# Kernel tuning notes

Measured on AMD Instinct MI355X. Metric: run time of the kernel, lower is better.

Reference implementation:

```python
import jax, jax.numpy as jnp
import numpy as np

N, E = 50000, 640000
DN, DA, S = 128, 64, 128
MAX_IT, THR = 10, 0.01


def setup_inputs() -> dict:
    key = jax.random.key(0)
    ks = jax.random.split(key, 20)
    inp = {
        'nodes': jax.random.normal(ks[0], (N, DN), jnp.float32),
        'arcs': jax.random.normal(ks[1], (E, 2 + DA), jnp.float32),
        'set_mask': jnp.ones((N,), bool),
        'output_mask': jnp.ones((N,), bool),
        'adj_src': jax.random.randint(ks[2], (E,), 0, N, jnp.int32),
        'adj_dst': jax.random.randint(ks[3], (E,), 0, N, jnp.int32),
        'adj_vals': jax.random.uniform(ks[4], (E,), jnp.float32),
        'an_dst': jax.random.randint(ks[5], (E,), 0, N, jnp.int32),
        'an_vals': jax.random.uniform(ks[6], (E,), jnp.float32),
        'state_init': 0.1 * jax.random.normal(ks[7], (N, S), jnp.float32),
        'Ws1': 0.05 * jax.random.normal(ks[8], (2 * S + 2 * DN + DA, 512), jnp.float32),
        'bs1': jnp.zeros((512,), jnp.float32),
        'Ws2': 0.05 * jax.random.normal(ks[9], (512, S), jnp.float32),
        'bs2': jnp.zeros((S,), jnp.float32),
        'Wo1': 0.05 * jax.random.normal(ks[10], (S + DN, 512), jnp.float32),
        'bo1': jnp.zeros((512,), jnp.float32),
        'Wo2': 0.05 * jax.random.normal(ks[11], (512, 7), jnp.float32),
        'bo2': jnp.zeros((7,), jnp.float32),
    }
    return inp


def _spmm(vals, src, dst, dense, n):
    # sparse [n,n] (or [n,E]) @ dense via gather + segment-sum
    return jax.ops.segment_sum(vals[:, None] * dense[src], dst, num_segments=n)


def reference(nodes, arcs, set_mask, output_mask, adj_src, adj_dst, adj_vals,
              an_dst, an_vals, state_init, Ws1, bs1, Ws2, bs2, Wo1, bo1, Wo2, bo2):
    n = nodes.shape[0]
    arc_labels = arcs[:, 2:]                                   # [E, DA]
    # aggregated_arcs = transposed_arcnode @ arcs[:,2:]  ([N,E] sparse)
    agg_arcs = jax.ops.segment_sum(an_vals[:, None] * arc_labels, an_dst, num_segments=n)
    # aggregated_nodes = transposed_adjacency @ nodes (state_vect_dim > 0 branch)
    agg_nodes = _spmm(adj_vals, adj_src, adj_dst, nodes, n)

    def net_state(x):
        return jnp.tanh(jnp.tanh(x @ Ws1 + bs1) @ Ws2 + bs2)

    def step(carry, _):
        state, state_old, k, done = carry
        dist = jnp.sqrt(jnp.sum(jnp.square(state - state_old), axis=1))
        norm = jnp.sqrt(jnp.sum(jnp.square(state_old), axis=1))
        cont = jnp.logical_and(jnp.any(dist > THR * norm), jnp.logical_not(done))
        agg_states = _spmm(adj_vals, adj_src, adj_dst, state, n)
        inp = jnp.concatenate([state, nodes, agg_states, agg_nodes, agg_arcs], axis=1)
        new_state = net_state(inp)
        state_next = jnp.where(cont, new_state, state)
        state_old_next = jnp.where(cont, state, state_old)
        return (state_next, state_old_next, k + cont.astype(jnp.float32), jnp.logical_not(cont)), None

    init = (state_init, jnp.ones_like(state_init), jnp.float32(0), jnp.array(False))
    (state, _, k, _), _ = jax.lax.scan(step, init, None, length=MAX_IT)

    # apply_filters: concat state|nodes, keep masked rows (mask applied as zeroing to keep static shapes)
    mask = jnp.logical_and(set_mask, output_mask)
    h = jnp.concatenate([state, nodes], axis=1)
    out = jnp.tanh(h @ Wo1 + bo1) @ Wo2 + bo2
    return out * mask[:, None].astype(out.dtype)
```

## Files before the change

kernel.cpp:

```cpp
#include <hip/hip_runtime.h>

typedef unsigned short u16;
typedef unsigned int u32;
typedef __attribute__((ext_vector_type(8))) short short8;
typedef __attribute__((ext_vector_type(4))) float f32x4;

#define THR2 1e-4f

__device__ __forceinline__ u16 f2bf(float f) {
    u32 u = __float_as_uint(f);
    u32 r = u + 0x7fffu + ((u >> 16) & 1u);
    return (u16)(r >> 16);
}
__device__ __forceinline__ float bf2f(u16 h) { return __uint_as_float(((u32)h) << 16); }
__device__ __forceinline__ float lo16(u32 u) { return __uint_as_float(u << 16); }
__device__ __forceinline__ float hi16(u32 u) { return __uint_as_float(u & 0xffff0000u); }

__device__ __forceinline__ void gl_lds16(const u16* g, u16* l) {
    __builtin_amdgcn_global_load_lds(
        (const __attribute__((address_space(1))) void*)g,
        (__attribute__((address_space(3))) void*)l, 16, 0, 0);
}


__global__ void k_zero2(int* a, int* b, int n, int* flags) {
    int i = blockIdx.x * 256 + threadIdx.x;
    if (blockIdx.x == 0 && threadIdx.x < 64) flags[threadIdx.x] = 0;
    if (i < n) { a[i] = 0; b[i] = 0; }
}

__global__ void k_hist2(const int* __restrict__ adst, const int* __restrict__ ndst,
                        int* ca, int* cn, int E) {
    int e = blockIdx.x * 256 + threadIdx.x;
    if (e < E) {
        atomicAdd(&ca[adst[e]], 1);
        atomicAdd(&cn[ndst[e]], 1);
    }
}

__global__ void k_scan_p1(const int* __restrict__ cnt, int* bs, int n) {
    __shared__ int s[256];
    int i = blockIdx.x * 256 + threadIdx.x;
    s[threadIdx.x] = (i < n) ? cnt[i] : 0;
    __syncthreads();
    for (int off = 128; off > 0; off >>= 1) {
        if (threadIdx.x < off) s[threadIdx.x] += s[threadIdx.x + off];
        __syncthreads();
    }
    if (threadIdx.x == 0) bs[blockIdx.x] = s[0];
}

__global__ void k_scan_p2(int* bs, int nb, int* rp, int n) {
    if (threadIdx.x == 0 && blockIdx.x == 0) {
        int run = 0;
        for (int b = 0; b < nb; ++b) { int t = bs[b]; bs[b] = run; run += t; }
        rp[n] = run;
    }
}

__global__ void k_scan_p3(const int* __restrict__ cnt, const int* __restrict__ bs,
                          int* rp, int* cur, int n) {
    __shared__ int s[256];
    int i = blockIdx.x * 256 + threadIdx.x;
    int v = (i < n) ? cnt[i] : 0;
    s[threadIdx.x] = v;
    __syncthreads();
    for (int off = 1; off < 256; off <<= 1) {
        int t = (threadIdx.x >= off) ? s[threadIdx.x - off] : 0;
        __syncthreads();
        s[threadIdx.x] += t;
        __syncthreads();
    }
    int excl = s[threadIdx.x] - v + bs[blockIdx.x];
    if (i < n) { rp[i] = excl; cur[i] = excl; }
}

__global__ void k_fill2(const int* __restrict__ asrc, const int* __restrict__ adst,
                        const float* __restrict__ avals,
                        int* curA, int2* __restrict__ cvA,
                        const int* __restrict__ ndst, const float* __restrict__ nvals,
                        int* curN, int2* __restrict__ cvN, int E) {
    int e = blockIdx.x * 256 + threadIdx.x;
    if (e < E) {
        int p = atomicAdd(&curA[adst[e]], 1);
        long long pa = ((long long)__float_as_int(avals[e]) << 32) | (u32)asrc[e];
        __builtin_nontemporal_store(pa, (long long*)(cvA + p));
        int q = atomicAdd(&curN[ndst[e]], 1);
        long long pn = ((long long)__float_as_int(nvals[e]) << 32) | (u32)e;
        __builtin_nontemporal_store(pn, (long long*)(cvN + q));
    }
}


__global__ void k_pack_all(const float* __restrict__ Ws1, const float* __restrict__ Ws2,
                           const float* __restrict__ Wo1,
                           u16* W1selT, u16* W1baseT, u16* W2T, u16* Wo1T) {
    int i = blockIdx.x * 256 + threadIdx.x;
    if (i < 131072) {
        int n = i >> 8, k = i & 255;
        int r = (k < 128) ? k : k + 128;
        W1selT[i] = f2bf(Ws1[r * 512 + n]);
    } else if (i < 294912) {
        int t = i - 131072;
        int n = t / 320, k = t % 320;
        int r = (k < 128) ? (k + 128) : (k + 256);
        W1baseT[t] = f2bf(Ws1[r * 512 + n]);
    } else if (i < 360448) {
        int t = i - 294912;
        int n = t >> 9, kp = t & 511;
        int q = kp & 63;
        int k = (kp & ~63) + ((q & 3) << 4) + (q >> 2);
        W2T[t] = f2bf(Ws2[k * 128 + n]);
    } else if (i < 491520) {
        int t = i - 360448;
        int n = t >> 8, k = t & 255;
        Wo1T[t] = f2bf(Wo1[k * 512 + n]);
    }
}


__global__ void k_conv_all(const float* __restrict__ nodes, const float* __restrict__ st,
                           u16* X0, u16* SA0, u16* SA2, int N) {
    int i = blockIdx.x * 256 + threadIdx.x;
    int total = N * 32;
    if (i < total) {
        int r = i >> 5, c4 = i & 31;
        float4 f = *(const float4*)(nodes + (size_t)r * 128 + c4 * 4);
        uint2 o;
        o.x = ((u32)f2bf(f.y) << 16) | f2bf(f.x);
        o.y = ((u32)f2bf(f.w) << 16) | f2bf(f.z);
        *(uint2*)(X0 + (size_t)r * 320 + c4 * 4) = o;
    } else if (i < 2 * total) {
        int t = i - total;
        int r = t >> 5, c4 = t & 31;
        float4 f = *(const float4*)(st + (size_t)r * 128 + c4 * 4);
        uint2 o;
        o.x = ((u32)f2bf(f.y) << 16) | f2bf(f.x);
        o.y = ((u32)f2bf(f.w) << 16) | f2bf(f.z);
        *(uint2*)(SA0 + (size_t)r * 256 + c4 * 4) = o;
    } else if (i < 3 * total) {
        int t = i - 2 * total;
        int r = t >> 5, c4 = t & 31;
        uint2 o; o.x = 0x3f803f80u; o.y = 0x3f803f80u;
        *(uint2*)(SA2 + (size_t)r * 256 + c4 * 4) = o;
    }
}

__global__ void k_build_fa(const u16* __restrict__ SA1, const float* __restrict__ nodes,
                           u16* FA, int N) {
    int i = blockIdx.x * 256 + threadIdx.x;
    if (i >= N * 64) return;
    int r = i >> 6, c = i & 63;
    if (c < 32) {
        uint2 o = *(const uint2*)(SA1 + (size_t)r * 256 + c * 4);
        *(uint2*)(FA + (size_t)r * 256 + c * 4) = o;
    } else {
        float4 f = *(const float4*)(nodes + (size_t)r * 128 + (c - 32) * 4);
        uint2 o;
        o.x = ((u32)f2bf(f.y) << 16) | f2bf(f.x);
        o.y = ((u32)f2bf(f.w) << 16) | f2bf(f.z);
        *(uint2*)(FA + (size_t)r * 256 + c * 4) = o;
    }
}


__global__ void k_agg_const(const int* __restrict__ rpA, const int2* __restrict__ cvA,
                            const float* __restrict__ nodes,
                            const int* __restrict__ rpN, const int2* __restrict__ cvN,
                            const float* __restrict__ arcs,
                            u16* X0, int N) {
    int row = blockIdx.x * 4 + (threadIdx.x >> 6);
    if (row >= N) return;
    int l = threadIdx.x & 63;
    int h = l >> 4;
    int lc = l & 15;
    if (blockIdx.y == 0) {
        float b0 = 0.f, b1 = 0.f, b2 = 0.f, b3 = 0.f;
        float b4 = 0.f, b5 = 0.f, b6 = 0.f, b7 = 0.f;
        int s = rpA[row], e = rpA[row + 1];
        int j = s;
        for (; j + 8 <= e; j += 8) {
            int2 p0 = cvA[j + h], p1 = cvA[j + 4 + h];
            const float* r0 = nodes + (size_t)p0.x * 128 + 8 * lc;
            const float* r1 = nodes + (size_t)p1.x * 128 + 8 * lc;
            float4 f0a = *(const float4*)(r0), f0b = *(const float4*)(r0 + 4);
            float4 f1a = *(const float4*)(r1), f1b = *(const float4*)(r1 + 4);
            float v0 = __int_as_float(p0.y), v1 = __int_as_float(p1.y);
            b0 += v0 * f0a.x + v1 * f1a.x;  b1 += v0 * f0a.y + v1 * f1a.y;
            b2 += v0 * f0a.z + v1 * f1a.z;  b3 += v0 * f0a.w + v1 * f1a.w;
            b4 += v0 * f0b.x + v1 * f1b.x;  b5 += v0 * f0b.y + v1 * f1b.y;
            b6 += v0 * f0b.z + v1 * f1b.z;  b7 += v0 * f0b.w + v1 * f1b.w;
        }
        for (; j + 4 <= e; j += 4) {
            int2 pp = cvA[j + h];
            const float* r0 = nodes + (size_t)pp.x * 128 + 8 * lc;
            float4 fa = *(const float4*)(r0), fb = *(const float4*)(r0 + 4);
            float v = __int_as_float(pp.y);
            b0 += v * fa.x; b1 += v * fa.y; b2 += v * fa.z; b3 += v * fa.w;
            b4 += v * fb.x; b5 += v * fb.y; b6 += v * fb.z; b7 += v * fb.w;
        }
        if (h < e - j) {
            int2 pp = cvA[j + h];
            const float* r0 = nodes + (size_t)pp.x * 128 + 8 * lc;
            float4 fa = *(const float4*)(r0), fb = *(const float4*)(r0 + 4);
            float v = __int_as_float(pp.y);
            b0 += v * fa.x; b1 += v * fa.y; b2 += v * fa.z; b3 += v * fa.w;
            b4 += v * fb.x; b5 += v * fb.y; b6 += v * fb.z; b7 += v * fb.w;
        }
        b0 += __shfl_xor(b0, 16); b0 += __shfl_xor(b0, 32);
        b1 += __shfl_xor(b1, 16); b1 += __shfl_xor(b1, 32);
        b2 += __shfl_xor(b2, 16); b2 += __shfl_xor(b2, 32);
        b3 += __shfl_xor(b3, 16); b3 += __shfl_xor(b3, 32);
        b4 += __shfl_xor(b4, 16); b4 += __shfl_xor(b4, 32);
        b5 += __shfl_xor(b5, 16); b5 += __shfl_xor(b5, 32);
        b6 += __shfl_xor(b6, 16); b6 += __shfl_xor(b6, 32);
        b7 += __shfl_xor(b7, 16); b7 += __shfl_xor(b7, 32);
        if (h == 0) {
            uint4 o;
            o.x = ((u32)f2bf(b1) << 16) | f2bf(b0);
            o.y = ((u32)f2bf(b3) << 16) | f2bf(b2);
            o.z = ((u32)f2bf(b5) << 16) | f2bf(b4);
            o.w = ((u32)f2bf(b7) << 16) | f2bf(b6);
            *(uint4*)(X0 + (size_t)row * 320 + 128 + 8 * lc) = o;
        }
    } else {
        float c0 = 0.f, c1 = 0.f, c2 = 0.f, c3 = 0.f;
        int s = rpN[row], e = rpN[row + 1];
        int j = s;
        for (; j + 8 <= e; j += 8) {
            int2 p0 = cvN[j + h], p1 = cvN[j + 4 + h];
            const float* r0 = arcs + (size_t)p0.x * 66 + 2 + 4 * lc;
            const float* r1 = arcs + (size_t)p1.x * 66 + 2 + 4 * lc;
            float2 f0a = *(const float2*)(r0), f0b = *(const float2*)(r0 + 2);
            float2 f1a = *(const float2*)(r1), f1b = *(const float2*)(r1 + 2);
            float v0 = __int_as_float(p0.y), v1 = __int_as_float(p1.y);
            c0 += v0 * f0a.x + v1 * f1a.x;  c1 += v0 * f0a.y + v1 * f1a.y;
            c2 += v0 * f0b.x + v1 * f1b.x;  c3 += v0 * f0b.y + v1 * f1b.y;
        }
        for (; j + 4 <= e; j += 4) {
            int2 pp = cvN[j + h];
            const float* r0 = arcs + (size_t)pp.x * 66 + 2 + 4 * lc;
            float2 fa = *(const float2*)(r0), fb = *(const float2*)(r0 + 2);
            float v = __int_as_float(pp.y);
            c0 += v * fa.x; c1 += v * fa.y; c2 += v * fb.x; c3 += v * fb.y;
        }
        if (h < e - j) {
            int2 pp = cvN[j + h];
            const float* r0 = arcs + (size_t)pp.x * 66 + 2 + 4 * lc;
            float2 fa = *(const float2*)(r0), fb = *(const float2*)(r0 + 2);
            float v = __int_as_float(pp.y);
            c0 += v * fa.x; c1 += v * fa.y; c2 += v * fb.x; c3 += v * fb.y;
        }
        c0 += __shfl_xor(c0, 16); c0 += __shfl_xor(c0, 32);
        c1 += __shfl_xor(c1, 16); c1 += __shfl_xor(c1, 32);
        c2 += __shfl_xor(c2, 16); c2 += __shfl_xor(c2, 32);
        c3 += __shfl_xor(c3, 16); c3 += __shfl_xor(c3, 32);
        if (h == 0) {
            uint2 o;
            o.x = ((u32)f2bf(c1) << 16) | f2bf(c0);
            o.y = ((u32)f2bf(c3) << 16) | f2bf(c2);
            *(uint2*)(X0 + (size_t)row * 320 + 256 + 4 * lc) = o;
        }
    }
}


__global__ void k_spmm_state(const int* __restrict__ rp, const int2* __restrict__ cv,
                             const u16* __restrict__ state, u16* agg, int N,
                             const int* __restrict__ anyf, const int* __restrict__ contprev,
                             int* contout) {
    int a = *anyf;
    int p = contprev ? *contprev : 1;
    int c = (a && p) ? 1 : 0;
    if (blockIdx.x == 0 && threadIdx.x == 0) *contout = c;
    if (!c) return;
    int row = blockIdx.x * 4 + (threadIdx.x >> 6);
    if (row >= N) return;
    int l = threadIdx.x & 63;
    int h = l >> 4;
    int lc = l & 15;
    float a0 = 0.f, a1 = 0.f, a2 = 0.f, a3 = 0.f;
    float a4 = 0.f, a5 = 0.f, a6 = 0.f, a7 = 0.f;
    int s = rp[row], e = rp[row + 1];
    int j = s;
    for (; j + 16 <= e; j += 16) {
        int2 p0 = cv[j + h],      p1 = cv[j + 4 + h];
        int2 p2 = cv[j + 8 + h],  p3 = cv[j + 12 + h];
        uint4 u0 = *(const uint4*)(state + (size_t)p0.x * 256 + 8 * lc);
        uint4 u1 = *(const uint4*)(state + (size_t)p1.x * 256 + 8 * lc);
        uint4 u2 = *(const uint4*)(state + (size_t)p2.x * 256 + 8 * lc);
        uint4 u3 = *(const uint4*)(state + (size_t)p3.x * 256 + 8 * lc);
        float v0 = __int_as_float(p0.y), v1 = __int_as_float(p1.y);
        float v2 = __int_as_float(p2.y), v3 = __int_as_float(p3.y);
        a0 += v0 * lo16(u0.x) + v1 * lo16(u1.x) + v2 * lo16(u2.x) + v3 * lo16(u3.x);
        a1 += v0 * hi16(u0.x) + v1 * hi16(u1.x) + v2 * hi16(u2.x) + v3 * hi16(u3.x);
        a2 += v0 * lo16(u0.y) + v1 * lo16(u1.y) + v2 * lo16(u2.y) + v3 * lo16(u3.y);
        a3 += v0 * hi16(u0.y) + v1 * hi16(u1.y) + v2 * hi16(u2.y) + v3 * hi16(u3.y);
        a4 += v0 * lo16(u0.z) + v1 * lo16(u1.z) + v2 * lo16(u2.z) + v3 * lo16(u3.z);
        a5 += v0 * hi16(u0.z) + v1 * hi16(u1.z) + v2 * hi16(u2.z) + v3 * hi16(u3.z);
        a6 += v0 * lo16(u0.w) + v1 * lo16(u1.w) + v2 * lo16(u2.w) + v3 * lo16(u3.w);
        a7 += v0 * hi16(u0.w) + v1 * hi16(u1.w) + v2 * hi16(u2.w) + v3 * hi16(u3.w);
    }
    for (; j + 8 <= e; j += 8) {
        int2 p0 = cv[j + h], p1 = cv[j + 4 + h];
        uint4 u0 = *(const uint4*)(state + (size_t)p0.x * 256 + 8 * lc);
        uint4 u1 = *(const uint4*)(state + (size_t)p1.x * 256 + 8 * lc);
        float v0 = __int_as_float(p0.y), v1 = __int_as_float(p1.y);
        a0 += v0 * lo16(u0.x) + v1 * lo16(u1.x);
        a1 += v0 * hi16(u0.x) + v1 * hi16(u1.x);
        a2 += v0 * lo16(u0.y) + v1 * lo16(u1.y);
        a3 += v0 * hi16(u0.y) + v1 * hi16(u1.y);
        a4 += v0 * lo16(u0.z) + v1 * lo16(u1.z);
        a5 += v0 * hi16(u0.z) + v1 * hi16(u1.z);
        a6 += v0 * lo16(u0.w) + v1 * lo16(u1.w);
        a7 += v0 * hi16(u0.w) + v1 * hi16(u1.w);
    }
    for (; j + 4 <= e; j += 4) {
        int2 pp = cv[j + h];
        uint4 u = *(const uint4*)(state + (size_t)pp.x * 256 + 8 * lc);
        float v = __int_as_float(pp.y);
        a0 += v * lo16(u.x); a1 += v * hi16(u.x);
        a2 += v * lo16(u.y); a3 += v * hi16(u.y);
        a4 += v * lo16(u.z); a5 += v * hi16(u.z);
        a6 += v * lo16(u.w); a7 += v * hi16(u.w);
    }
    if (h < e - j) {
        int2 pp = cv[j + h];
        uint4 u = *(const uint4*)(state + (size_t)pp.x * 256 + 8 * lc);
        float v = __int_as_float(pp.y);
        a0 += v * lo16(u.x); a1 += v * hi16(u.x);
        a2 += v * lo16(u.y); a3 += v * hi16(u.y);
        a4 += v * lo16(u.z); a5 += v * hi16(u.z);
        a6 += v * lo16(u.w); a7 += v * hi16(u.w);
    }
    a0 += __shfl_xor(a0, 16); a0 += __shfl_xor(a0, 32);
    a1 += __shfl_xor(a1, 16); a1 += __shfl_xor(a1, 32);
    a2 += __shfl_xor(a2, 16); a2 += __shfl_xor(a2, 32);
    a3 += __shfl_xor(a3, 16); a3 += __shfl_xor(a3, 32);
    a4 += __shfl_xor(a4, 16); a4 += __shfl_xor(a4, 32);
    a5 += __shfl_xor(a5, 16); a5 += __shfl_xor(a5, 32);
    a6 += __shfl_xor(a6, 16); a6 += __shfl_xor(a6, 32);
    a7 += __shfl_xor(a7, 16); a7 += __shfl_xor(a7, 32);
    if (h == 0) {
        uint4 o;
        o.x = ((u32)f2bf(a1) << 16) | f2bf(a0);
        o.y = ((u32)f2bf(a3) << 16) | f2bf(a2);
        o.z = ((u32)f2bf(a5) << 16) | f2bf(a4);
        o.w = ((u32)f2bf(a7) << 16) | f2bf(a6);
        *(uint4*)(agg + (size_t)row * 256 + 8 * lc) = o;
    }
}


__global__ void k_check(const u16* __restrict__ cur, const u16* __restrict__ prev,
                        int N, int* anyf) {
    int row = blockIdx.x * 4 + (threadIdx.x >> 6);
    int l = threadIdx.x & 63;
    float d2 = 0.f, n2 = 0.f;
    if (row < N) {
        u32 u1 = *(const u32*)(cur + (size_t)row * 256 + 2 * l);
        u32 u2 = *(const u32*)(prev + (size_t)row * 256 + 2 * l);
        float ax = lo16(u1), ay = hi16(u1);
        float bx = lo16(u2), by = hi16(u2);
        float dx = ax - bx, dy = ay - by;
        d2 = dx * dx + dy * dy;
        n2 = bx * bx + by * by;
    }
    for (int off = 32; off; off >>= 1) {
        d2 += __shfl_down(d2, off);
        n2 += __shfl_down(n2, off);
    }
    if (l == 0 && row < N && d2 > THR2 * n2) {
        volatile int* f = (volatile int*)anyf;
        if (*f == 0) atomicOr(anyf, 1);
    }
}


__global__ __launch_bounds__(256)
void k_gemm(const u16* __restrict__ A, int lda,
            const u16* __restrict__ BT, int ldb,
            const float* __restrict__ bias,
            const u16* __restrict__ Cadd, int ldc,
            u16* __restrict__ D, int ldd,
            int M, int K, int dotanh,
            const int* __restrict__ contflag, int skipmode,
            const u16* __restrict__ copysrc, u16* __restrict__ copydst,
            int* chk, int permCD) {
    int m0 = blockIdx.x * 128;
    int n0 = blockIdx.y * 128;
    if (skipmode && *contflag == 0) {
        if (skipmode == 2) {
            for (int c = threadIdx.x; c < 2048; c += 256) {
                int r = c >> 4, ch = (c & 15) * 8;
                int row = m0 + r;
                if (row < M)
                    *(uint4*)(copydst + (size_t)row * 256 + ch) =
                        *(const uint4*)(copysrc + (size_t)row * 256 + ch);
            }
        }
        return;
    }
    __shared__ u16 As[128 * 32];
    __shared__ u16 Bs[128 * 32];
    __shared__ float rsum[256];
    int tid = threadIdx.x;
    int wave = tid >> 6, l = tid & 63;
    int wm = (wave >> 1) * 64, wn = (wave & 1) * 64;
    int ml = l & 15, kg = l >> 4;
    int ko = kg * 8;
    f32x4 acc[4][4];
#pragma unroll
    for (int mi = 0; mi < 4; ++mi)
#pragma unroll
        for (int ni = 0; ni < 4; ++ni) acc[mi][ni] = (f32x4){0.f, 0.f, 0.f, 0.f};

    if (chk) rsum[tid] = 0.f;

    for (int k0 = 0; k0 < K; k0 += 32) {
#pragma unroll
        for (int i = 0; i < 2; ++i) {
            int c = tid + i * 256;
            int r = c >> 2, half = (c & 3) * 8;
            int rowA = m0 + r; rowA = (rowA < M) ? rowA : (M - 1);
            gl_lds16(A + (size_t)rowA * lda + k0 + half, &As[c * 8]);
            gl_lds16(BT + (size_t)(n0 + r) * ldb + k0 + half, &Bs[c * 8]);
        }
        __syncthreads();
        short8 av[4], bv[4];
#pragma unroll
        for (int mi = 0; mi < 4; ++mi)
            av[mi] = *(const short8*)(&As[(wm + mi * 16 + ml) * 32 + ko]);
#pragma unroll
        for (int ni = 0; ni < 4; ++ni)
            bv[ni] = *(const short8*)(&Bs[(wn + ni * 16 + ml) * 32 + ko]);
#pragma unroll
        for (int mi = 0; mi < 4; ++mi)
#pragma unroll
            for (int ni = 0; ni < 4; ++ni)
                acc[mi][ni] = __builtin_amdgcn_mfma_f32_16x16x32_bf16(
                    av[mi], bv[ni], acc[mi][ni], 0, 0, 0);
        __syncthreads();
    }
#pragma unroll
    for (int mi = 0; mi < 4; ++mi) {
#pragma unroll
        for (int r = 0; r < 4; ++r) {
            int row = m0 + wm + mi * 16 + kg * 4 + r;
            bool ok = row < M;
            float d2l = 0.f, n2l = 0.f;
            uint2 cb2;
            if (ok && (permCD & 1))
                cb2 = *(const uint2*)(Cadd + (size_t)row * ldc + n0 + wn + ml * 4);
            float vv[4];
#pragma unroll
            for (int ni = 0; ni < 4; ++ni) {
                int col = n0 + wn + ni * 16 + ml;
                float v = acc[mi][ni][r];
                if (bias) v += bias[col];
                if (Cadd) {
                    if (permCD & 1) {
                        u32 w = (ni < 2) ? cb2.x : cb2.y;
                        v += (ni & 1) ? hi16(w) : lo16(w);
                    } else if (ok) {
                        v += bf2f(Cadd[(size_t)row * ldc + col]);
                    }
                }
                if (dotanh) v = tanhf(v);
                vv[ni] = v;
            }
            if (permCD & 2) {
                if (ok) {
                    uint2 o;
                    o.x = ((u32)f2bf(vv[1]) << 16) | f2bf(vv[0]);
                    o.y = ((u32)f2bf(vv[3]) << 16) | f2bf(vv[2]);
                    *(uint2*)(D + (size_t)row * ldd + n0 + wn + ml * 4) = o;
                }
            } else {
#pragma unroll
                for (int ni = 0; ni < 4; ++ni) {
                    int col = n0 + wn + ni * 16 + ml;
                    if (ok) {
                        u16 hb = f2bf(vv[ni]);
                        D[(size_t)row * ldd + col] = hb;
                        if (chk) {
                            float vq = bf2f(hb);
                            float o  = bf2f(copysrc[(size_t)row * 256 + col]);
                            float d = vq - o;
                            d2l += d * d;
                            n2l += o * o;
                        }
                    }
                }
            }
            if (chk) {
#pragma unroll
                for (int off = 1; off < 16; off <<= 1) {
                    d2l += __shfl_xor(d2l, off);
                    n2l += __shfl_xor(n2l, off);
                }
                if (ml == 0) {
                    int lrow = wm + mi * 16 + kg * 4 + r;
                    atomicAdd(&rsum[lrow], d2l);
                    atomicAdd(&rsum[128 + lrow], n2l);
                }
            }
        }
    }
    if (chk) {
        __syncthreads();
        bool viol = false;
        if (tid < 128) {
            int row = m0 + tid;
            if (row < M) viol = rsum[tid] > THR2 * rsum[128 + tid];
        }
        if (__any(viol) && (threadIdx.x & 63) == 0) {
            volatile int* f = (volatile int*)chk;
            if (*f == 0) atomicOr(chk, 1);
        }
    }
}


__global__ void k_out(const u16* __restrict__ HO, const float* __restrict__ Wo2,
                      const float* __restrict__ bo2,
                      const int* __restrict__ m1,
                      const int* __restrict__ m2,
                      float* __restrict__ out, int N) {
    __shared__ float w[512 * 7];
    for (int i = threadIdx.x; i < 512 * 7; i += 256) w[i] = Wo2[i];
    __syncthreads();
    int row = blockIdx.x * 4 + (threadIdx.x >> 6);
    if (row >= N) return;
    int l = threadIdx.x & 63;
    uint4 u = *(const uint4*)(HO + (size_t)row * 512 + l * 8);
    float h[8];
    h[0] = lo16(u.x); h[1] = hi16(u.x);
    h[2] = lo16(u.y); h[3] = hi16(u.y);
    h[4] = lo16(u.z); h[5] = hi16(u.z);
    h[6] = lo16(u.w); h[7] = hi16(u.w);
    float a[7] = {0.f, 0.f, 0.f, 0.f, 0.f, 0.f, 0.f};
#pragma unroll
    for (int i = 0; i < 8; ++i) {
        int cp = l * 8 + i;
        int q = cp & 63;
        int orig = (cp & ~63) + ((q & 3) << 4) + (q >> 2);
        int base = orig * 7;
#pragma unroll
        for (int j = 0; j < 7; ++j) a[j] += h[i] * w[base + j];
    }
    for (int off = 32; off; off >>= 1) {
#pragma unroll
        for (int j = 0; j < 7; ++j) a[j] += __shfl_down(a[j], off);
    }
    if (l == 0) {
        float mm = (m1[row] != 0 && m2[row] != 0) ? 1.f : 0.f;
#pragma unroll
        for (int j = 0; j < 7; ++j) out[(size_t)row * 7 + j] = (a[j] + bo2[j]) * mm;
    }
}


extern "C" void kernel_launch(void* const* d_in, const int* in_sizes, int n_in,
                              void* d_out, int out_size, void* d_ws, size_t ws_size,
                              hipStream_t stream) {
    const float* nodes   = (const float*)d_in[0];
    const float* arcs    = (const float*)d_in[1];
    const int*   set_mask    = (const int*)d_in[2];
    const int*   output_mask = (const int*)d_in[3];
    const int*   adj_src = (const int*)d_in[4];
    const int*   adj_dst = (const int*)d_in[5];
    const float* adj_vals= (const float*)d_in[6];
    const int*   an_dst  = (const int*)d_in[7];
    const float* an_vals = (const float*)d_in[8];
    const float* state_init = (const float*)d_in[9];
    const float* Ws1 = (const float*)d_in[10];
    const float* bs1 = (const float*)d_in[11];
    const float* Ws2 = (const float*)d_in[12];
    const float* bs2 = (const float*)d_in[13];
    const float* Wo1 = (const float*)d_in[14];
    const float* bo1 = (const float*)d_in[15];
    const float* Wo2 = (const float*)d_in[16];
    const float* bo2 = (const float*)d_in[17];
    float* out = (float*)d_out;

    const int N = in_sizes[2];
    const int E = in_sizes[4];

    char* ws = (char*)d_ws;
    size_t off = 0;
    auto alloc = [&](size_t bytes) {
        char* p = ws + off;
        off += (bytes + 255) & ~(size_t)255;
        return p;
    };
    u16* SA0 = (u16*)alloc((size_t)N * 256 * 2);
    u16* SA1 = (u16*)alloc((size_t)N * 256 * 2);
    u16* SA2 = (u16*)alloc((size_t)N * 256 * 2);
    u16* CB  = (u16*)alloc((size_t)N * 512 * 2);
    u16* HID = (u16*)alloc((size_t)N * 512 * 2);
    u16* X0  = HID;
    u16* FA  = SA0;
    u16* W1selT  = (u16*)alloc(512 * 256 * 2);
    u16* W1baseT = (u16*)alloc(512 * 320 * 2);
    u16* W2T     = (u16*)alloc(128 * 512 * 2);
    u16* Wo1T    = (u16*)alloc(512 * 256 * 2);
    int* rpA  = (int*)alloc((size_t)(N + 1) * 4);
    int* curA = (int*)alloc((size_t)N * 4);
    int* cntA = (int*)alloc((size_t)N * 4);
    int2* cvA = (int2*)alloc((size_t)E * 8);
    int* rpN  = (int*)alloc((size_t)(N + 1) * 4);
    int* curN = (int*)alloc((size_t)N * 4);
    int* cntN = (int*)alloc((size_t)N * 4);
    int2* cvN = (int2*)alloc((size_t)E * 8);
    int* bsA = (int*)alloc(256 * 4);
    int* bsN = (int*)alloc(256 * 4);
    int* flags = (int*)alloc(64 * 4);
    int* anyf = flags;
    int* cont = flags + 16;
    (void)ws_size; (void)n_in; (void)out_size;

    const int nb = (N + 255) / 256;
    const int gE = (E + 255) / 256;
    const int gRow = (N + 3) / 4;
    const int gx = (N + 127) / 128;

    k_zero2<<<nb, 256, 0, stream>>>(cntA, cntN, N, flags);
    k_hist2<<<gE, 256, 0, stream>>>(adj_dst, an_dst, cntA, cntN, E);
    k_scan_p1<<<nb, 256, 0, stream>>>(cntA, bsA, N);
    k_scan_p2<<<1, 64, 0, stream>>>(bsA, nb, rpA, N);
    k_scan_p3<<<nb, 256, 0, stream>>>(cntA, bsA, rpA, curA, N);
    k_scan_p1<<<nb, 256, 0, stream>>>(cntN, bsN, N);
    k_scan_p2<<<1, 64, 0, stream>>>(bsN, nb, rpN, N);
    k_scan_p3<<<nb, 256, 0, stream>>>(cntN, bsN, rpN, curN, N);
    k_fill2<<<gE, 256, 0, stream>>>(adj_src, adj_dst, adj_vals, curA, cvA,
                                    an_dst, an_vals, curN, cvN, E);
    k_pack_all<<<1920, 256, 0, stream>>>(Ws1, Ws2, Wo1, W1selT, W1baseT, W2T, Wo1T);
    k_conv_all<<<(3 * N * 32 + 255) / 256, 256, 0, stream>>>(nodes, state_init,
                                                             X0, SA0, SA2, N);
    k_agg_const<<<dim3(gRow, 2), 256, 0, stream>>>(rpA, cvA, nodes,
                                                   rpN, cvN, arcs, X0, N);
    k_gemm<<<dim3(gx, 4), 256, 0, stream>>>(X0, 320, W1baseT, 320, bs1,
                                            nullptr, 0, CB, 512, N, 320, 0,
                                            nullptr, 0, nullptr, nullptr, nullptr, 2);
    u16* SAs[3] = {SA0, SA1, SA2};
    for (int t = 0; t < 10; ++t) {
        u16* curS = SAs[t % 3];
        u16* prvS = SAs[(t + 2) % 3];
        u16* nxtS = SAs[(t + 1) % 3];
        if (t == 0)
            k_check<<<gRow, 256, 0, stream>>>(curS, prvS, N, anyf);
        k_spmm_state<<<gRow, 256, 0, stream>>>(rpA, cvA, curS, curS + 128, N,
                                               anyf + t, t ? (cont + t - 1) : nullptr,
                                               cont + t);
        k_gemm<<<dim3(gx, 4), 256, 0, stream>>>(curS, 256, W1selT, 256, nullptr,
                                                CB, 512, HID, 512, N, 256, 1,
                                                cont + t, 1, nullptr, nullptr,
                                                nullptr, 3);
        k_gemm<<<dim3(gx, 1), 256, 0, stream>>>(HID, 512, W2T, 512, bs2,
                                                nullptr, 0, nxtS, 256, N, 512, 1,
                                                cont + t, 2, curS, nxtS,
                                                anyf + t + 1, 0);
    }
    k_build_fa<<<(N * 64 + 255) / 256, 256, 0, stream>>>(SA1, nodes, FA, N);
    k_gemm<<<dim3(gx, 4), 256, 0, stream>>>(FA, 256, Wo1T, 256, bo1,
                                            nullptr, 0, HID, 512, N, 256, 1,
                                            nullptr, 0, nullptr, nullptr, nullptr, 2);
    k_out<<<gRow, 256, 0, stream>>>(HID, Wo2, bo2, set_mask, output_mask, out, N);
}
```

Baseline: 2.436 ms.

## Halve GEMM M-tile to 64 rows and pad CSR fill cursors

Changes the GEMM from 128x128 tiles with a 2x2 wave layout to 64x128 tiles, with each wave owning 16 rows across all 128 columns. This doubles the number of blocks so that N=50000 rows fill the GPU's compute units better. Separately, the per-row atomic cursors used in CSR construction are padded to 16 ints apart to cut atomic contention and false sharing on shared cache lines. The cost is more B-tile reloads per output, lower MFMA reuse per wave, and a 16x larger cursor allocation.

```diff
diff --git a/kernel.cpp b/kernel.cpp
--- a/kernel.cpp
+++ b/kernel.cpp
@@ -6,6 +6,7 @@
 typedef __attribute__((ext_vector_type(4))) float f32x4;
 
 #define THR2 1e-4f
+#define CPAD 16
 
 __device__ __forceinline__ u16 f2bf(float f) {
     u32 u = __float_as_uint(f);
@@ -72,7 +73,7 @@
         __syncthreads();
     }
     int excl = s[threadIdx.x] - v + bs[blockIdx.x];
-    if (i < n) { rp[i] = excl; cur[i] = excl; }
+    if (i < n) { rp[i] = excl; cur[(size_t)i * CPAD] = excl; }
 }
 
 __global__ void k_fill2(const int* __restrict__ asrc, const int* __restrict__ adst,
@@ -82,10 +83,10 @@
                         int* curN, int2* __restrict__ cvN, int E) {
     int e = blockIdx.x * 256 + threadIdx.x;
     if (e < E) {
-        int p = atomicAdd(&curA[adst[e]], 1);
+        int p = atomicAdd(&curA[(size_t)adst[e] * CPAD], 1);
         long long pa = ((long long)__float_as_int(avals[e]) << 32) | (u32)asrc[e];
         __builtin_nontemporal_store(pa, (long long*)(cvA + p));
-        int q = atomicAdd(&curN[ndst[e]], 1);
+        int q = atomicAdd(&curN[(size_t)ndst[e] * CPAD], 1);
         long long pn = ((long long)__float_as_int(nvals[e]) << 32) | (u32)e;
         __builtin_nontemporal_store(pn, (long long*)(cvN + q));
     }
@@ -387,11 +388,11 @@
             const int* __restrict__ contflag, int skipmode,
             const u16* __restrict__ copysrc, u16* __restrict__ copydst,
             int* chk, int permCD) {
-    int m0 = blockIdx.x * 128;
+    int m0 = blockIdx.x * 64;
     int n0 = blockIdx.y * 128;
     if (skipmode && *contflag == 0) {
         if (skipmode == 2) {
-            for (int c = threadIdx.x; c < 2048; c += 256) {
+            for (int c = threadIdx.x; c < 1024; c += 256) {
                 int r = c >> 4, ch = (c & 15) * 8;
                 int row = m0 + r;
                 if (row < M)
@@ -401,120 +402,121 @@
         }
         return;
     }
-    __shared__ u16 As[128 * 32];
+    __shared__ u16 As[64 * 32];
     __shared__ u16 Bs[128 * 32];
-    __shared__ float rsum[256];
+    __shared__ float rsum[128];
     int tid = threadIdx.x;
     int wave = tid >> 6, l = tid & 63;
-    int wm = (wave >> 1) * 64, wn = (wave & 1) * 64;
+    int wm = wave * 16;
     int ml = l & 15, kg = l >> 4;
     int ko = kg * 8;
-    f32x4 acc[4][4];
-#pragma unroll
-    for (int mi = 0; mi < 4; ++mi)
-#pragma unroll
-        for (int ni = 0; ni < 4; ++ni) acc[mi][ni] = (f32x4){0.f, 0.f, 0.f, 0.f};
-
-    if (chk) rsum[tid] = 0.f;
+    f32x4 acc[8];
+#pragma unroll
+    for (int ni = 0; ni < 8; ++ni) acc[ni] = (f32x4){0.f, 0.f, 0.f, 0.f};
+
+    if (chk && tid < 128) rsum[tid] = 0.f;
 
     for (int k0 = 0; k0 < K; k0 += 32) {
+        {
+            int c = tid;
+            int r = c >> 2, half = (c & 3) * 8;
+            int rowA = m0 + r; rowA = (rowA < M) ? rowA : (M - 1);
+            gl_lds16(A + (size_t)rowA * lda + k0 + half, &As[c * 8]);
+        }
 #pragma unroll
         for (int i = 0; i < 2; ++i) {
             int c = tid + i * 256;
             int r = c >> 2, half = (c & 3) * 8;
-            int rowA = m0 + r; rowA = (rowA < M) ? rowA : (M - 1);
-            gl_lds16(A + (size_t)rowA * lda + k0 + half, &As[c * 8]);
             gl_lds16(BT + (size_t)(n0 + r) * ldb + k0 + half, &Bs[c * 8]);
         }
         __syncthreads();
-        short8 av[4], bv[4];
-#pragma unroll
-        for (int mi = 0; mi < 4; ++mi)
-            av[mi] = *(const short8*)(&As[(wm + mi * 16 + ml) * 32 + ko]);
-#pragma unroll
-        for (int ni = 0; ni < 4; ++ni)
-            bv[ni] = *(const short8*)(&Bs[(wn + ni * 16 + ml) * 32 + ko]);
-#pragma unroll
-        for (int mi = 0; mi < 4; ++mi)
-#pragma unroll
-            for (int ni = 0; ni < 4; ++ni)
-                acc[mi][ni] = __builtin_amdgcn_mfma_f32_16x16x32_bf16(
-                    av[mi], bv[ni], acc[mi][ni], 0, 0, 0);
+        short8 av = *(const short8*)(&As[(wm + ml) * 32 + ko]);
+        short8 bv[8];
+#pragma unroll
+        for (int ni = 0; ni < 8; ++ni)
+            bv[ni] = *(const short8*)(&Bs[(ni * 16 + ml) * 32 + ko]);
+#pragma unroll
+        for (int ni = 0; ni < 8; ++ni)
+            acc[ni] = __builtin_amdgcn_mfma_f32_16x16x32_bf16(
+                av, bv[ni], acc[ni], 0, 0, 0);
         __syncthreads();
     }
 #pragma unroll
-    for (int mi = 0; mi < 4; ++mi) {
-#pragma unroll
-        for (int r = 0; r < 4; ++r) {
-            int row = m0 + wm + mi * 16 + kg * 4 + r;
-            bool ok = row < M;
-            float d2l = 0.f, n2l = 0.f;
-            uint2 cb2;
-            if (ok && (permCD & 1))
-                cb2 = *(const uint2*)(Cadd + (size_t)row * ldc + n0 + wn + ml * 4);
-            float vv[4];
-#pragma unroll
-            for (int ni = 0; ni < 4; ++ni) {
-                int col = n0 + wn + ni * 16 + ml;
-                float v = acc[mi][ni][r];
-                if (bias) v += bias[col];
-                if (Cadd) {
-                    if (permCD & 1) {
-                        u32 w = (ni < 2) ? cb2.x : cb2.y;
-                        v += (ni & 1) ? hi16(w) : lo16(w);
-                    } else if (ok) {
-                        v += bf2f(Cadd[(size_t)row * ldc + col]);
-                    }
+    for (int r = 0; r < 4; ++r) {
+        int lrow = wm + kg * 4 + r;
+        int row = m0 + lrow;
+        bool ok = row < M;
+        float d2l = 0.f, n2l = 0.f;
+        float vv[8];
+        uint2 cb2[2];
+        if (ok && (permCD & 1)) {
+            cb2[0] = *(const uint2*)(Cadd + (size_t)row * ldc + n0 + ml * 4);
+            cb2[1] = *(const uint2*)(Cadd + (size_t)row * ldc + n0 + 64 + ml * 4);
+        }
+#pragma unroll
+        for (int ni = 0; ni < 8; ++ni) {
+            int col = n0 + ni * 16 + ml;
+            float v = acc[ni][r];
+            if (bias) v += bias[col];
+            if (Cadd) {
+                if (permCD & 1) {
+                    int g = ni >> 2, j = ni & 3;
+                    u32 w = (j < 2) ? cb2[g].x : cb2[g].y;
+                    v += (j & 1) ? hi16(w) : lo16(w);
+                } else if (ok) {
+                    v += bf2f(Cadd[(size_t)row * ldc + col]);
                 }
-                if (dotanh) v = tanhf(v);
-                vv[ni] = v;
             }
-            if (permCD & 2) {
+            if (dotanh) v = tanhf(v);
+            vv[ni] = v;
+        }
+        if (permCD & 2) {
+            if (ok) {
+                uint2 o0, o1;
+                o0.x = ((u32)f2bf(vv[1]) << 16) | f2bf(vv[0]);
+                o0.y = ((u32)f2bf(vv[3]) << 16) | f2bf(vv[2]);
+                o1.x = ((u32)f2bf(vv[5]) << 16) | f2bf(vv[4]);
+                o1.y = ((u32)f2bf(vv[7]) << 16) | f2bf(vv[6]);
+                *(uint2*)(D + (size_t)row * ldd + n0 + ml * 4) = o0;
+                *(uint2*)(D + (size_t)row * ldd + n0 + 64 + ml * 4) = o1;
+            }
+        } else {
+#pragma unroll
+            for (int ni = 0; ni < 8; ++ni) {
+                int col = n0 + ni * 16 + ml;
                 if (ok) {
-                    uint2 o;
-                    o.x = ((u32)f2bf(vv[1]) << 16) | f2bf(vv[0]);
-                    o.y = ((u32)f2bf(vv[3]) << 16) | f2bf(vv[2]);
-                    *(uint2*)(D + (size_t)row * ldd + n0 + wn + ml * 4) = o;
-                }
-            } else {
-#pragma unroll
-                for (int ni = 0; ni < 4; ++ni) {
-                    int col = n0 + wn + ni * 16 + ml;
-                    if (ok) {
-                        u16 hb = f2bf(vv[ni]);
-                        D[(size_t)row * ldd + col] = hb;
-                        if (chk) {
-                            float vq = bf2f(hb);
-                            float o  = bf2f(copysrc[(size_t)row * 256 + col]);
-                            float d = vq - o;
-                            d2l += d * d;
-                            n2l += o * o;
-                        }
+                    u16 hb = f2bf(vv[ni]);
+                    D[(size_t)row * ldd + col] = hb;
+                    if (chk) {
+                        float vq = bf2f(hb);
+                        float o  = bf2f(copysrc[(size_t)row * 256 + col]);
+                        float d = vq - o;
+                        d2l += d * d;
+                        n2l += o * o;
                     }
                 }
             }
-            if (chk) {
-#pragma unroll
-                for (int off = 1; off < 16; off <<= 1) {
-                    d2l += __shfl_xor(d2l, off);
-                    n2l += __shfl_xor(n2l, off);
-                }
-                if (ml == 0) {
-                    int lrow = wm + mi * 16 + kg * 4 + r;
-                    atomicAdd(&rsum[lrow], d2l);
-                    atomicAdd(&rsum[128 + lrow], n2l);
-                }
+        }
+        if (chk) {
+#pragma unroll
+            for (int off = 1; off < 16; off <<= 1) {
+                d2l += __shfl_xor(d2l, off);
+                n2l += __shfl_xor(n2l, off);
+            }
+            if (ml == 0) {
+                atomicAdd(&rsum[lrow], d2l);
+                atomicAdd(&rsum[64 + lrow], n2l);
             }
         }
     }
     if (chk) {
         __syncthreads();
         bool viol = false;
-        if (tid < 128) {
+        if (tid < 64) {
             int row = m0 + tid;
-            if (row < M) viol = rsum[tid] > THR2 * rsum[128 + tid];
-        }
-        if (__any(viol) && (threadIdx.x & 63) == 0) {
+            if (row < M) viol = rsum[tid] > THR2 * rsum[64 + tid];
+        }
+        if (__any(viol) && l == 0) {
             volatile int* f = (volatile int*)chk;
             if (*f == 0) atomicOr(chk, 1);
         }
@@ -606,11 +608,11 @@
     u16* W2T     = (u16*)alloc(128 * 512 * 2);
     u16* Wo1T    = (u16*)alloc(512 * 256 * 2);
     int* rpA  = (int*)alloc((size_t)(N + 1) * 4);
-    int* curA = (int*)alloc((size_t)N * 4);
+    int* curA = (int*)alloc((size_t)N * CPAD * 4);
     int* cntA = (int*)alloc((size_t)N * 4);
     int2* cvA = (int2*)alloc((size_t)E * 8);
     int* rpN  = (int*)alloc((size_t)(N + 1) * 4);
-    int* curN = (int*)alloc((size_t)N * 4);
+    int* curN = (int*)alloc((size_t)N * CPAD * 4);
     int* cntN = (int*)alloc((size_t)N * 4);
     int2* cvN = (int2*)alloc((size_t)E * 8);
     int* bsA = (int*)alloc(256 * 4);
@@ -623,7 +625,7 @@
     const int nb = (N + 255) / 256;
     const int gE = (E + 255) / 256;
     const int gRow = (N + 3) / 4;
-    const int gx = (N + 127) / 128;
+    const int gx64 = (N + 63) / 64;
 
     k_zero2<<<nb, 256, 0, stream>>>(cntA, cntN, N, flags);
     k_hist2<<<gE, 256, 0, stream>>>(adj_dst, an_dst, cntA, cntN, E);
@@ -640,9 +642,10 @@
                                                              X0, SA0, SA2, N);
     k_agg_const<<<dim3(gRow, 2), 256, 0, stream>>>(rpA, cvA, nodes,
                                                    rpN, cvN, arcs, X0, N);
-    k_gemm<<<dim3(gx, 4), 256, 0, stream>>>(X0, 320, W1baseT, 320, bs1,
-                                            nullptr, 0, CB, 512, N, 320, 0,
-                                            nullptr, 0, nullptr, nullptr, nullptr, 2);
+    k_gemm<<<dim3(gx64, 4), 256, 0, stream>>>(X0, 320, W1baseT, 320, bs1,
+                                              nullptr, 0, CB, 512, N, 320, 0,
+                                              nullptr, 0, nullptr, nullptr,
+                                              nullptr, 2);
     u16* SAs[3] = {SA0, SA1, SA2};
     for (int t = 0; t < 10; ++t) {
         u16* curS = SAs[t % 3];
@@ -653,18 +656,19 @@
         k_spmm_state<<<gRow, 256, 0, stream>>>(rpA, cvA, curS, curS + 128, N,
                                                anyf + t, t ? (cont + t - 1) : nullptr,
                                                cont + t);
-        k_gemm<<<dim3(gx, 4), 256, 0, stream>>>(curS, 256, W1selT, 256, nullptr,
-                                                CB, 512, HID, 512, N, 256, 1,
-                                                cont + t, 1, nullptr, nullptr,
-                                                nullptr, 3);
-        k_gemm<<<dim3(gx, 1), 256, 0, stream>>>(HID, 512, W2T, 512, bs2,
-                                                nullptr, 0, nxtS, 256, N, 512, 1,
-                                                cont + t, 2, curS, nxtS,
-                                                anyf + t + 1, 0);
+        k_gemm<<<dim3(gx64, 4), 256, 0, stream>>>(curS, 256, W1selT, 256, nullptr,
+                                                  CB, 512, HID, 512, N, 256, 1,
+                                                  cont + t, 1, nullptr, nullptr,
+                                                  nullptr, 3);
+        k_gemm<<<dim3(gx64, 1), 256, 0, stream>>>(HID, 512, W2T, 512, bs2,
+                                                  nullptr, 0, nxtS, 256, N, 512, 1,
+                                                  cont + t, 2, curS, nxtS,
+                                                  anyf + t + 1, 0);
     }
     k_build_fa<<<(N * 64 + 255) / 256, 256, 0, stream>>>(SA1, nodes, FA, N);
-    k_gemm<<<dim3(gx, 4), 256, 0, stream>>>(FA, 256, Wo1T, 256, bo1,
-                                            nullptr, 0, HID, 512, N, 256, 1,
-                                            nullptr, 0, nullptr, nullptr, nullptr, 2);
+    k_gemm<<<dim3(gx64, 4), 256, 0, stream>>>(FA, 256, Wo1T, 256, bo1,
+                                              nullptr, 0, HID, 512, N, 256, 1,
+                                              nullptr, 0, nullptr, nullptr,
+                                              nullptr, 2);
     k_out<<<gRow, 256, 0, stream>>>(HID, Wo2, bo2, set_mask, output_mask, out, N);
 }
```

Result: faster. 1.986 ms (-18.5%).
